# Kernel optimization log

Measured on AMD Instinct MI355X. Metric: run time of the kernel, lower is better.

Reference implementation:

```python
import jax, jax.numpy as jnp
import numpy as np

B, T, IN, H, C = 64, 256, 512, 1024, 128

def _uniform(key, shape, scale):
    return jax.random.uniform(key, shape, jnp.float32, -scale, scale)

def setup_inputs() -> dict:
    key = jax.random.key(0)
    ks = jax.random.split(key, 12)
    s = 1.0 / np.sqrt(H)
    return {
        "xs": jax.random.normal(ks[0], (B, T, IN), jnp.float32),
        "W_ih0": _uniform(ks[1], (4 * H, IN), s),
        "W_hh0": _uniform(ks[2], (4 * H, H), s),
        "b_ih0": _uniform(ks[3], (4 * H,), s),
        "b_hh0": _uniform(ks[4], (4 * H,), s),
        "W_ih1": _uniform(ks[5], (4 * H, H), s),
        "W_hh1": _uniform(ks[6], (4 * H, H), s),
        "b_ih1": _uniform(ks[7], (4 * H,), s),
        "b_hh1": _uniform(ks[8], (4 * H,), s),
        "W_cls": _uniform(ks[9], (C, H), 1.0 / np.sqrt(H)),
        "b_cls": _uniform(ks[10], (C,), 1.0 / np.sqrt(H)),
    }

def _lstm_cell(x, h, c, W_ih, W_hh, b_ih, b_hh):
    # gates: [B, 4H], torch LSTMCell order i, f, g, o
    g = x @ W_ih.T + b_ih + h @ W_hh.T + b_hh
    i, f, gg, o = jnp.split(g, 4, axis=-1)
    c_new = jax.nn.sigmoid(f) * c + jax.nn.sigmoid(i) * jnp.tanh(gg)
    h_new = jax.nn.sigmoid(o) * jnp.tanh(c_new)
    return h_new, c_new

def reference(xs, W_ih0, W_hh0, b_ih0, b_hh0, W_ih1, W_hh1, b_ih1, b_hh1, W_cls, b_cls):
    batch = xs.shape[0]
    z = jnp.zeros((batch, H), xs.dtype)

    def step(carry, x_t):
        h0, c0, h1, c1 = carry
        h0, c0 = _lstm_cell(x_t, h0, c0, W_ih0, W_hh0, b_ih0, b_hh0)
        l0 = h0 @ W_cls.T + b_cls
        h1, c1 = _lstm_cell(h0, h1, c1, W_ih1, W_hh1, b_ih1, b_hh1)
        l1 = h1 @ W_cls.T + b_cls
        return (h0, c0, h1, c1), jnp.stack([l0, l1])  # [L=2, B, C]

    xs_t = jnp.swapaxes(xs[:, -T:, :], 0, 1)  # [T, B, IN]
    _, logits = jax.lax.scan(step, (z, z, z, z), xs_t)  # [T, L, B, C]
    # torch stacks the t-major, layer-minor list along dim=2 -> [B, C, T*L]
    return jnp.transpose(logits, (2, 3, 0, 1)).reshape(batch, C, T * 2)
```

## Files before the change

### kernel.cpp

```cpp
#include <hip/hip_runtime.h>

#define BB  64
#define TT  256
#define INF 512
#define HH  1024
#define CC  128

typedef __attribute__((ext_vector_type(8))) short bf16x8;
typedef __attribute__((ext_vector_type(4))) float f32x4;
typedef unsigned long long ull_t;
typedef unsigned short u16;

#define W0_LD 1544
#define W1_LD 2056
#define WC_LD 1032
#define GSC_OFF (16*W0_LD + 16*W1_LD + 16*WC_LD)
#define SMEM_BYTES (GSC_OFF*2 + 2*(4*16*17)*4 + 64)

#define HBUF (BB*HH)
#define BAR_BYTES 65536

#define AGENT __HIP_MEMORY_SCOPE_AGENT
#define RLX   __ATOMIC_RELAXED

__device__ __forceinline__ u16 f2bf(float f) {
    union { float f; unsigned u; } v; v.f = f;
    unsigned r = v.u + 0x7fffu + ((v.u >> 16) & 1u);
    return (u16)(r >> 16);
}
__device__ __forceinline__ float sigm(float x) { return 1.f / (1.f + __expf(-x)); }

#define MFMA(a,b,c) __builtin_amdgcn_mfma_f32_16x16x32_bf16((a),(b),(c),0,0,0)

template<bool PLAIN>
__device__ __forceinline__ bf16x8 ld_pair(const u16* slotbase, int bb, int ar) {
    union { ull_t u[2]; bf16x8 v; } x;
    const u16* p0 = slotbase + (bb << 8) + (ar << 2);
    if constexpr (PLAIN) {
        x.u[0] = *(const ull_t*)p0;
        x.u[1] = *(const ull_t*)(p0 + 256);
    } else {
        x.u[0] = __hip_atomic_load((const ull_t*)p0,         RLX, AGENT);
        x.u[1] = __hip_atomic_load((const ull_t*)(p0 + 256), RLX, AGENT);
    }
    return x.v;
}

#define POLL3(nF0, nF1, nFC) do { \
        const unsigned _n0 = (unsigned)(nF0), _n1 = (unsigned)(nF1), _nc = (unsigned)(nFC); \
        float _z = 1.f; \
        for (;;) { \
            bool _ok = true; \
            if (_n0) { \
                ull_t _a = __hip_atomic_load(f0p + (lane << 1),     RLX, AGENT); \
                ull_t _b = __hip_atomic_load(f0p + (lane << 1) + 1, RLX, AGENT); \
                _ok &= ((unsigned)_a >= _n0) && ((unsigned)(_a >> 32) >= _n0) \
                    && ((unsigned)_b >= _n0) && ((unsigned)(_b >> 32) >= _n0); \
            } \
            if (_n1) { \
                ull_t _a = __hip_atomic_load(f1p + (lane << 1),     RLX, AGENT); \
                ull_t _b = __hip_atomic_load(f1p + (lane << 1) + 1, RLX, AGENT); \
                _ok &= ((unsigned)_a >= _n1) && ((unsigned)(_a >> 32) >= _n1) \
                    && ((unsigned)_b >= _n1) && ((unsigned)(_b >> 32) >= _n1); \
            } \
            if (_nc && lane < 16) { \
                ull_t _a = __hip_atomic_load(fcp + lane, RLX, AGENT); \
                _ok &= ((unsigned)_a >= _nc) && ((unsigned)(_a >> 32) >= _nc); \
            } \
            if (__all(_ok)) break; \
            _Pragma("unroll 16") \
            for (int _i = 0; _i < 256; ++_i) _z = __builtin_fmaf(_z, 0.99999988f, 1e-9f); \
            asm volatile("" :: "v"(_z)); \
        } \
        asm volatile("" ::: "memory"); \
    } while (0)

template<int DEPTH, bool PLAIN>
__global__ __launch_bounds__(576, 1)
void lstm_persist(const float* __restrict__ xs,
                  const float* __restrict__ Wih0, const float* __restrict__ Whh0,
                  const float* __restrict__ bih0, const float* __restrict__ bhh0,
                  const float* __restrict__ Wih1, const float* __restrict__ Whh1,
                  const float* __restrict__ bih1, const float* __restrict__ bhh1,
                  const float* __restrict__ Wcls, const float* __restrict__ bcls,
                  float* __restrict__ out,
                  u16* __restrict__ hws,
                  unsigned* __restrict__ bar)
{
    extern __shared__ char smem[];
    u16* W0s = (u16*)smem;
    u16* W1s = W0s + 16*W0_LD;
    u16* WCs = W1s + 16*W1_LD;
    float* gsc0 = (float*)(smem + GSC_OFF*2);
    float* gsc1 = gsc0 + 4*16*17;
    unsigned* scnt = (unsigned*)(gsc1 + 4*16*17);

    const int blk   = blockIdx.x;
    const int tid   = threadIdx.x;
    const int wave  = tid >> 6;
    const int lane  = tid & 63;
    const int col16 = lane & 15;
    const int kgrp  = (lane >> 4) << 3;

    u16* ring0 = hws;
    u16* ring1 = hws + (size_t)DEPTH*HBUF;
    const ull_t* f0p = (const ull_t*)(bar + (blk & 7)*256);
    const ull_t* f1p = (const ull_t*)(bar + 2048 + (blk & 7)*256);
    const ull_t* fcp = (const ull_t*)(bar + 4096 + (blk & 7)*64);

#define SLOT(x) ((unsigned)(((x) + 2) % DEPTH))

    if (tid < 2) scnt[tid] = 0;
    for (int i = tid; i < 16*1536; i += 576) {
        int r = i / 1536, k = i - r*1536;
        int gr = 4*blk + (r & 3) + HH*(r >> 2);
        float v = (k < HH) ? Whh0[gr*HH + k] : Wih0[gr*INF + (k - HH)];
        W0s[r*W0_LD + k] = f2bf(v);
    }
    for (int i = tid; i < 16*2048; i += 576) {
        int r = i >> 11, k = i & 2047;
        int gr = 4*blk + (r & 3) + HH*(r >> 2);
        float v = (k < HH) ? Wih1[gr*HH + k] : Whh1[gr*HH + (k - HH)];
        W1s[r*W1_LD + k] = f2bf(v);
    }
    if (PLAIN || blk < 32) {
        int cb = (blk & 7) << 4;
        for (int i = tid; i < 16*1024; i += 576) {
            int r = i >> 10, k = i & 1023;
            WCs[r*WC_LD + k] = f2bf(Wcls[(cb + r)*HH + k]);
        }
    }
    __syncthreads();

    if (wave == 8) {
        const u16*  wcp   = WCs + col16*WC_LD + kgrp;
        const float biasc = bcls[((blk & 7) << 4) + col16];
        const int cc = ((blk & 7) << 4) + col16;
        const int cstart = PLAIN ? (blk >> 5) : 0;
        const int cstep  = PLAIN ? 8 : 1;
        const int R      = PLAIN ? ((blk & 31) >> 3) : (blk >> 3);
        const int arow2  = (R << 4) + col16;
        if (PLAIN || blk < 32) {
            for (int c = cstart; c < TT/8; c += cstep) {
                POLL3(0, 8*c + 8, 0);
                union { float2 f2[8]; f32x4 f4[4]; } o[4];
                #pragma unroll
                for (int tt = 0; tt < 8; ++tt) {
                    const int t = 8*c + tt;
                    const u16* s0 = ring0 + (size_t)SLOT(t)*HBUF;
                    const u16* s1 = ring1 + (size_t)SLOT(t)*HBUF;
                    f32x4 a0 = { biasc, biasc, biasc, biasc }, a1 = { 0.f, 0.f, 0.f, 0.f };
                    f32x4 b0 = { biasc, biasc, biasc, biasc }, b1 = { 0.f, 0.f, 0.f, 0.f };
                    #pragma unroll 4
                    for (int kc = 0; kc < 32; ++kc) {
                        const int bb = (kgrp >> 2) + (kc << 3);
                        const bf16x8 w  = *(const bf16x8*)(wcp + (kc << 5));
                        const bf16x8 x0 = ld_pair<PLAIN>(s0, bb, arow2);
                        const bf16x8 x1 = ld_pair<PLAIN>(s1, bb, arow2);
                        if (kc & 1) { a1 = MFMA(x0, w, a1); b1 = MFMA(x1, w, b1); }
                        else        { a0 = MFMA(x0, w, a0); b0 = MFMA(x1, w, b0); }
                    }
                    #pragma unroll
                    for (int q = 0; q < 4; ++q)
                        o[q].f2[tt] = make_float2(a0[q] + a1[q], b0[q] + b1[q]);
                }
                #pragma unroll
                for (int q = 0; q < 4; ++q) {
                    const int br = (R << 4) + ((lane >> 4) << 2) + q;
                    float* po = &out[(ull_t)(br*CC + cc)*(2*TT) + 16*c];
                    #pragma unroll
                    for (int s = 0; s < 4; ++s)
                        __builtin_nontemporal_store(o[q].f4[s], (f32x4*)(po + 4*s));
                }
                if (!PLAIN) {
                    asm volatile("s_waitcnt vmcnt(0)" ::: "memory");
                    if (lane < 8)
                        __hip_atomic_store(&bar[4096 + lane*64 + blk], (unsigned)(c + 1), RLX, AGENT);
                }
            }
        }
        return;
    }

    const int wv   = wave & 3;
    const int arow = (wv << 4) + col16;
    const int rloc = lane >> 2, jj = lane & 3;
    const u16* w0p = W0s + col16*W0_LD + kgrp;
    const u16* w1p = W1s + col16*W1_LD + kgrp;
    const int  grl = 4*blk + (col16 & 3) + HH*(col16 >> 2);

    if (wave < 4) {
        const float bias0 = bih0[grl] + bhh0[grl];
        float c0 = 0.f;
        f32x4 g0A = { bias0, bias0, bias0, bias0 }, g0B = { 0.f, 0.f, 0.f, 0.f };
        {
            const float* xp = xs + (arow*TT + 0)*INF + kgrp;
            #pragma unroll 4
            for (int kc = 0; kc < 16; ++kc) {
                const float4 x0 = *(const float4*)(xp + (kc << 5));
                const float4 x1 = *(const float4*)(xp + (kc << 5) + 4);
                bf16x8 a;
                a[0]=(short)f2bf(x0.x); a[1]=(short)f2bf(x0.y); a[2]=(short)f2bf(x0.z); a[3]=(short)f2bf(x0.w);
                a[4]=(short)f2bf(x1.x); a[5]=(short)f2bf(x1.y); a[6]=(short)f2bf(x1.z); a[7]=(short)f2bf(x1.w);
                const bf16x8 b = *(const bf16x8*)(w0p + ((32 + kc) << 5));
                if (kc & 1) g0B = MFMA(a, b, g0B); else g0A = MFMA(a, b, g0A);
            }
        }
        for (int t = 0; t < TT; ++t) {
            unsigned n1c = 0, ncc = 0;
            if constexpr (DEPTH <= TT) {
                if (t >= DEPTH) { n1c = (unsigned)(t - DEPTH + 1);
                                  ncc = (unsigned)((t - DEPTH)/8 + 1); }
            }
            POLL3(t, n1c, ncc);
            const u16* s0 = ring0 + (size_t)SLOT(t - 1)*HBUF;
            #pragma unroll 4
            for (int kc = 0; kc < 32; ++kc) {
                const int bb = (kgrp >> 2) + (kc << 3);
                const bf16x8 a = ld_pair<PLAIN>(s0, bb, arow);
                const bf16x8 b = *(const bf16x8*)(w0p + (kc << 5));
                if (kc & 1) g0B = MFMA(a, b, g0B); else g0A = MFMA(a, b, g0A);
            }
            #pragma unroll
            for (int qq = 0; qq < 4; ++qq)
                gsc0[wv*272 + (((lane >> 4) << 2) + qq)*17 + col16] = g0A[qq] + g0B[qq];
            asm volatile("s_waitcnt lgkmcnt(0)" ::: "memory");
            const float* g = gsc0 + wv*272 + rloc*17;
            const float ig = sigm(g[jj]), fg = sigm(g[4 + jj]);
            const float gt = tanhf(g[8 + jj]), og = sigm(g[12 + jj]);
            c0 = fg*c0 + ig*gt;
            unsigned v = f2bf(og * tanhf(c0));
            unsigned p = v | (__shfl_down(v, 1) << 16);
            ull_t all = ((ull_t)__shfl_down(p, 2) << 32) | (ull_t)p;
            if (jj == 0)
                __hip_atomic_store((ull_t*)(ring0 + (size_t)SLOT(t)*HBUF
                                            + (blk << 8) + (((wv << 4) + rloc) << 2)),
                                   all, RLX, AGENT);
            asm volatile("s_waitcnt vmcnt(0)" ::: "memory");
            {
                unsigned old = 0;
                if (lane == 0) old = atomicAdd(&scnt[0], 1u);
                old = (unsigned)__shfl((int)old, 0);
                if (old == 4u*(unsigned)t + 3u && lane < 8)
                    __hip_atomic_store(&bar[lane*256 + blk], (unsigned)(t + 1), RLX, AGENT);
            }
            if (t + 1 < TT) {
                g0A[0]=bias0; g0A[1]=bias0; g0A[2]=bias0; g0A[3]=bias0;
                g0B[0]=0.f;   g0B[1]=0.f;   g0B[2]=0.f;   g0B[3]=0.f;
                const float* xp = xs + (arow*TT + (t + 1))*INF + kgrp;
                #pragma unroll 4
                for (int kc = 0; kc < 16; ++kc) {
                    const float4 x0 = *(const float4*)(xp + (kc << 5));
                    const float4 x1 = *(const float4*)(xp + (kc << 5) + 4);
                    bf16x8 a;
                    a[0]=(short)f2bf(x0.x); a[1]=(short)f2bf(x0.y); a[2]=(short)f2bf(x0.z); a[3]=(short)f2bf(x0.w);
                    a[4]=(short)f2bf(x1.x); a[5]=(short)f2bf(x1.y); a[6]=(short)f2bf(x1.z); a[7]=(short)f2bf(x1.w);
                    const bf16x8 b = *(const bf16x8*)(w0p + ((32 + kc) << 5));
                    if (kc & 1) g0B = MFMA(a, b, g0B); else g0A = MFMA(a, b, g0A);
                }
            }
        }
    } else {
        const float bias1 = bih1[grl] + bhh1[grl];
        float c1 = 0.f;
        for (int t = 1; t <= TT; ++t) {
            unsigned ncc1 = 0;
            if constexpr (DEPTH <= TT) {
                if (t - 1 >= DEPTH) ncc1 = (unsigned)((t - 1 - DEPTH)/8 + 1);
            }
            POLL3(0, t - 1, ncc1);
            f32x4 g1A = { bias1, bias1, bias1, bias1 }, g1B = { 0.f, 0.f, 0.f, 0.f };
            const u16* s1 = ring1 + (size_t)SLOT(t - 2)*HBUF;
            #pragma unroll 4
            for (int kc = 0; kc < 32; ++kc) {
                const int bb = (kgrp >> 2) + (kc << 3);
                const bf16x8 a = ld_pair<PLAIN>(s1, bb, arow);
                const bf16x8 b = *(const bf16x8*)(w1p + ((32 + kc) << 5));
                if (kc & 1) g1B = MFMA(a, b, g1B); else g1A = MFMA(a, b, g1A);
            }
            POLL3(t, 0, 0);
            const u16* s0 = ring0 + (size_t)SLOT(t - 1)*HBUF;
            #pragma unroll 4
            for (int kc = 0; kc < 32; ++kc) {
                const int bb = (kgrp >> 2) + (kc << 3);
                const bf16x8 a = ld_pair<PLAIN>(s0, bb, arow);
                const bf16x8 b = *(const bf16x8*)(w1p + (kc << 5));
                if (kc & 1) g1B = MFMA(a, b, g1B); else g1A = MFMA(a, b, g1A);
            }
            #pragma unroll
            for (int qq = 0; qq < 4; ++qq)
                gsc1[wv*272 + (((lane >> 4) << 2) + qq)*17 + col16] = g1A[qq] + g1B[qq];
            asm volatile("s_waitcnt lgkmcnt(0)" ::: "memory");
            const float* g = gsc1 + wv*272 + rloc*17;
            const float ig = sigm(g[jj]), fg = sigm(g[4 + jj]);
            const float gt = tanhf(g[8 + jj]), og = sigm(g[12 + jj]);
            c1 = fg*c1 + ig*gt;
            unsigned v = f2bf(og * tanhf(c1));
            unsigned p = v | (__shfl_down(v, 1) << 16);
            ull_t all = ((ull_t)__shfl_down(p, 2) << 32) | (ull_t)p;
            if (jj == 0)
                __hip_atomic_store((ull_t*)(ring1 + (size_t)SLOT(t - 1)*HBUF
                                            + (blk << 8) + (((wv << 4) + rloc) << 2)),
                                   all, RLX, AGENT);
            asm volatile("s_waitcnt vmcnt(0)" ::: "memory");
            {
                unsigned old = 0;
                if (lane == 0) old = atomicAdd(&scnt[1], 1u);
                old = (unsigned)__shfl((int)old, 0);
                if (old == 4u*(unsigned)(t - 1) + 3u && lane < 8)
                    __hip_atomic_store(&bar[2048 + lane*256 + blk], (unsigned)t, RLX, AGENT);
            }
        }
    }
#undef SLOT
}

template<int DEPTH, bool PLAIN>
static void launch_tier(const float* xs, const float* Wih0, const float* Whh0,
                        const float* bih0, const float* bhh0,
                        const float* Wih1, const float* Whh1,
                        const float* bih1, const float* bhh1,
                        const float* Wcls, const float* bcls,
                        float* out, void* d_ws, hipStream_t stream) {
    u16* hws = (u16*)d_ws;
    size_t ringB = (size_t)DEPTH*HBUF*2;
    unsigned* bar = (unsigned*)((char*)d_ws + 2*ringB);
    (void)hipMemsetAsync(hws, 0, 2*(size_t)HBUF*2, stream);
    (void)hipMemsetAsync((char*)hws + ringB, 0, 2*(size_t)HBUF*2, stream);
    (void)hipMemsetAsync(bar, 0, BAR_BYTES, stream);
    (void)hipFuncSetAttribute((const void*)lstm_persist<DEPTH, PLAIN>,
                              hipFuncAttributeMaxDynamicSharedMemorySize, SMEM_BYTES);
    lstm_persist<DEPTH, PLAIN><<<dim3(256), dim3(576), SMEM_BYTES, stream>>>(
        xs, Wih0, Whh0, bih0, bhh0, Wih1, Whh1, bih1, bhh1, Wcls, bcls,
        out, hws, bar);
}

extern "C" void kernel_launch(void* const* d_in, const int* in_sizes, int n_in,
                              void* d_out, int out_size, void* d_ws, size_t ws_size,
                              hipStream_t stream) {
    const float* xs   = (const float*)d_in[0];
    const float* Wih0 = (const float*)d_in[1];
    const float* Whh0 = (const float*)d_in[2];
    const float* bih0 = (const float*)d_in[3];
    const float* bhh0 = (const float*)d_in[4];
    const float* Wih1 = (const float*)d_in[5];
    const float* Whh1 = (const float*)d_in[6];
    const float* bih1 = (const float*)d_in[7];
    const float* bhh1 = (const float*)d_in[8];
    const float* Wcls = (const float*)d_in[9];
    const float* bcls = (const float*)d_in[10];
    float* out = (float*)d_out;

    auto need = [](int depth) { return (size_t)2*depth*HBUF*2 + BAR_BYTES; };

    if (ws_size >= need(258))
        launch_tier<258, true >(xs,Wih0,Whh0,bih0,bhh0,Wih1,Whh1,bih1,bhh1,Wcls,bcls,out,d_ws,stream);
    else if (ws_size >= need(32))
        launch_tier< 32, false>(xs,Wih0,Whh0,bih0,bhh0,Wih1,Whh1,bih1,bhh1,Wcls,bcls,out,d_ws,stream);
    else if (ws_size >= need(16))
        launch_tier< 16, false>(xs,Wih0,Whh0,bih0,bhh0,Wih1,Whh1,bih1,bhh1,Wcls,bcls,out,d_ws,stream);
    else
        launch_tier<  8, false>(xs,Wih0,Whh0,bih0,bhh0,Wih1,Whh1,bih1,bhh1,Wcls,bcls,out,d_ws,stream);
}
```

Baseline: 4.168 ms.

## Add wave priorities, spinner wave, and shorter backoff for layer-0 critical path

Adds a tenth wave per block that spins on FMA work at lowest priority until layer 1 finishes. The apparent aim is to keep the CU's clocks or occupancy from dropping while the other waves poll. Layer-0 waves get raised priority around their critical compute and a shorter poll backoff, while the classifier and layer-1 waves run at lower priority. The extra wave takes VALU issue slots and power, and priority tuning could starve the dependent waves.

Result: no change. 4.231 ms (+1.5%).

```diff
diff --git a/kernel.cpp b/kernel.cpp
--- a/kernel.cpp
+++ b/kernel.cpp
@@ -31,6 +31,7 @@
 __device__ __forceinline__ float sigm(float x) { return 1.f / (1.f + __expf(-x)); }
 
 #define MFMA(a,b,c) __builtin_amdgcn_mfma_f32_16x16x32_bf16((a),(b),(c),0,0,0)
+#define PRIO(n) __builtin_amdgcn_s_setprio(n)
 
 template<bool PLAIN>
 __device__ __forceinline__ bf16x8 ld_pair(const u16* slotbase, int bb, int ar) {
@@ -46,7 +47,7 @@
     return x.v;
 }
 
-#define POLL3(nF0, nF1, nFC) do { \
+#define POLL3(nF0, nF1, nFC, BK) do { \
         const unsigned _n0 = (unsigned)(nF0), _n1 = (unsigned)(nF1), _nc = (unsigned)(nFC); \
         float _z = 1.f; \
         for (;;) { \
@@ -69,14 +70,14 @@
             } \
             if (__all(_ok)) break; \
             _Pragma("unroll 16") \
-            for (int _i = 0; _i < 256; ++_i) _z = __builtin_fmaf(_z, 0.99999988f, 1e-9f); \
+            for (int _i = 0; _i < (BK); ++_i) _z = __builtin_fmaf(_z, 0.99999988f, 1e-9f); \
             asm volatile("" :: "v"(_z)); \
         } \
         asm volatile("" ::: "memory"); \
     } while (0)
 
 template<int DEPTH, bool PLAIN>
-__global__ __launch_bounds__(576, 1)
+__global__ __launch_bounds__(640, 1)
 void lstm_persist(const float* __restrict__ xs,
                   const float* __restrict__ Wih0, const float* __restrict__ Whh0,
                   const float* __restrict__ bih0, const float* __restrict__ bhh0,
@@ -111,13 +112,13 @@
 #define SLOT(x) ((unsigned)(((x) + 2) % DEPTH))
 
     if (tid < 2) scnt[tid] = 0;
-    for (int i = tid; i < 16*1536; i += 576) {
+    for (int i = tid; i < 16*1536; i += 640) {
         int r = i / 1536, k = i - r*1536;
         int gr = 4*blk + (r & 3) + HH*(r >> 2);
         float v = (k < HH) ? Whh0[gr*HH + k] : Wih0[gr*INF + (k - HH)];
         W0s[r*W0_LD + k] = f2bf(v);
     }
-    for (int i = tid; i < 16*2048; i += 576) {
+    for (int i = tid; i < 16*2048; i += 640) {
         int r = i >> 11, k = i & 2047;
         int gr = 4*blk + (r & 3) + HH*(r >> 2);
         float v = (k < HH) ? Wih1[gr*HH + k] : Whh1[gr*HH + (k - HH)];
@@ -125,14 +126,28 @@
     }
     if (PLAIN || blk < 32) {
         int cb = (blk & 7) << 4;
-        for (int i = tid; i < 16*1024; i += 576) {
+        for (int i = tid; i < 16*1024; i += 640) {
             int r = i >> 10, k = i & 1023;
             WCs[r*WC_LD + k] = f2bf(Wcls[(cb + r)*HH + k]);
         }
     }
     __syncthreads();
 
+    if (wave == 9) {
+        PRIO(0);
+        const unsigned* myf1 = bar + 2048 + (blk & 7)*256 + blk;
+        float a = 1.0000001f, b = 0.99999988f;
+        for (;;) {
+            #pragma unroll 32
+            for (int i = 0; i < 4096; ++i) a = __builtin_fmaf(a, b, 1e-9f);
+            asm volatile("" :: "v"(a));
+            if (__hip_atomic_load(myf1, RLX, AGENT) >= (unsigned)TT) break;
+        }
+        return;
+    }
+
     if (wave == 8) {
+        PRIO(0);
         const u16*  wcp   = WCs + col16*WC_LD + kgrp;
         const float biasc = bcls[((blk & 7) << 4) + col16];
         const int cc = ((blk & 7) << 4) + col16;
@@ -142,7 +157,7 @@
         const int arow2  = (R << 4) + col16;
         if (PLAIN || blk < 32) {
             for (int c = cstart; c < TT/8; c += cstep) {
-                POLL3(0, 8*c + 8, 0);
+                POLL3(0, 8*c + 8, 0, 256);
                 union { float2 f2[8]; f32x4 f4[4]; } o[4];
                 #pragma unroll
                 for (int tt = 0; tt < 8; ++tt) {
@@ -212,7 +227,9 @@
                 if (t >= DEPTH) { n1c = (unsigned)(t - DEPTH + 1);
                                   ncc = (unsigned)((t - DEPTH)/8 + 1); }
             }
-            POLL3(t, n1c, ncc);
+            PRIO(1);
+            POLL3(t, n1c, ncc, 128);
+            PRIO(2);
             const u16* s0 = ring0 + (size_t)SLOT(t - 1)*HBUF;
             #pragma unroll 4
             for (int kc = 0; kc < 32; ++kc) {
@@ -244,6 +261,7 @@
                 if (old == 4u*(unsigned)t + 3u && lane < 8)
                     __hip_atomic_store(&bar[lane*256 + blk], (unsigned)(t + 1), RLX, AGENT);
             }
+            PRIO(1);
             if (t + 1 < TT) {
                 g0A[0]=bias0; g0A[1]=bias0; g0A[2]=bias0; g0A[3]=bias0;
                 g0B[0]=0.f;   g0B[1]=0.f;   g0B[2]=0.f;   g0B[3]=0.f;
@@ -268,7 +286,9 @@
             if constexpr (DEPTH <= TT) {
                 if (t - 1 >= DEPTH) ncc1 = (unsigned)((t - 1 - DEPTH)/8 + 1);
             }
-            POLL3(0, t - 1, ncc1);
+            PRIO(0);
+            POLL3(0, t - 1, ncc1, 256);
+            PRIO(1);
             f32x4 g1A = { bias1, bias1, bias1, bias1 }, g1B = { 0.f, 0.f, 0.f, 0.f };
             const u16* s1 = ring1 + (size_t)SLOT(t - 2)*HBUF;
             #pragma unroll 4
@@ -278,7 +298,9 @@
                 const bf16x8 b = *(const bf16x8*)(w1p + ((32 + kc) << 5));
                 if (kc & 1) g1B = MFMA(a, b, g1B); else g1A = MFMA(a, b, g1A);
             }
-            POLL3(t, 0, 0);
+            PRIO(0);
+            POLL3(t, 0, 0, 256);
+            PRIO(1);
             const u16* s0 = ring0 + (size_t)SLOT(t - 1)*HBUF;
             #pragma unroll 4
             for (int kc = 0; kc < 32; ++kc) {
@@ -330,7 +352,7 @@
     (void)hipMemsetAsync(bar, 0, BAR_BYTES, stream);
     (void)hipFuncSetAttribute((const void*)lstm_persist<DEPTH, PLAIN>,
                               hipFuncAttributeMaxDynamicSharedMemorySize, SMEM_BYTES);
-    lstm_persist<DEPTH, PLAIN><<<dim3(256), dim3(576), SMEM_BYTES, stream>>>(
+    lstm_persist<DEPTH, PLAIN><<<dim3(256), dim3(640), SMEM_BYTES, stream>>>(
         xs, Wih0, Whh0, bih0, bhh0, Wih1, Whh1, bih1, bhh1, Wcls, bcls,
         out, hws, bar);
 }
```
